# Kernel tuning notes

Hardware: AMD Instinct MI355X
Metric: run time of the kernel (lower is better)

## Reference

```python
import jax, jax.numpy as jnp
import numpy as np

NUM_SEGMENTS = 100000  # number of cycle slots (max cycle id + 1)


def setup_inputs() -> dict:
    key = jax.random.key(0)
    k1, k2, k3 = jax.random.split(key, 3)
    x = jax.random.randint(k1, (100000,), 0, 22, dtype=jnp.int64)
    atom_to_cycle = jax.random.randint(k2, (2, 600000), 0, NUM_SEGMENTS, dtype=jnp.int64)
    emb_weight = jax.random.normal(k3, (22, 128), dtype=jnp.float32)  # Embedding(22, hidden_dim)
    return {"x": x, "atom_to_cycle": atom_to_cycle, "emb_weight": emb_weight}


def reference(x, atom_to_cycle, emb_weight):
    # x: [N] int atom codes; atom_to_cycle: [2, E]; emb_weight: [22, D]
    h = emb_weight[x]                       # [N, D] embedding lookup
    gathered = h[atom_to_cycle[0]]          # [E, D] gather by atom index
    # scatter_sum over cycle ids -> [NUM_SEGMENTS, D]
    out = jax.ops.segment_sum(gathered, atom_to_cycle[1], num_segments=NUM_SEGMENTS)
    return out
```

## Files before the change

kernel.cpp:

```cpp
#include <hip/hip_runtime.h>
#include <stdint.h>

#define KCODES 22
#define KW     12

typedef int   int2v   __attribute__((ext_vector_type(2)));
typedef int   int4v   __attribute__((ext_vector_type(4)));
typedef float float4v __attribute__((ext_vector_type(4)));

#define BSHIFT   7
#define BROWS    128
#define BCAP     4096
#define EPT      8
#define CHUNK    2048
#define MAXBUCK  1024

__global__ __launch_bounds__(256) void bin_edges(
        const int* __restrict__ a2c, const int* __restrict__ x,
        uint32_t* __restrict__ gcur, uint16_t* __restrict__ bins,
        int E, int nbuck) {
    __shared__ uint32_t lcnt[MAXBUCK];
    __shared__ uint32_t lbase[MAXBUCK];
    const int tid = threadIdx.x;
    for (int b = tid; b < nbuck; b += 256) lcnt[b] = 0;
    __syncthreads();

    const int base = blockIdx.x * CHUNK + tid * EPT;
    int atoms[EPT] __attribute__((aligned(16)));
    int cycs[EPT]  __attribute__((aligned(16)));
    if (((E & 3) == 0) && (base + EPT <= E)) {
        *(int4v*)(atoms + 0) = __builtin_nontemporal_load((const int4v*)(a2c + base));
        *(int4v*)(atoms + 4) = __builtin_nontemporal_load((const int4v*)(a2c + base) + 1);
        *(int4v*)(cycs + 0)  = __builtin_nontemporal_load((const int4v*)(a2c + E + base));
        *(int4v*)(cycs + 4)  = __builtin_nontemporal_load((const int4v*)(a2c + E + base) + 1);
    } else {
#pragma unroll
        for (int j = 0; j < EPT; ++j) {
            int e = base + j;
            atoms[j] = (e < E) ? a2c[e] : 0;
            cycs[j]  = (e < E) ? a2c[E + e] : -1;
        }
    }

    uint16_t val[EPT], bk[EPT], rk[EPT];
#pragma unroll
    for (int j = 0; j < EPT; ++j) {
        if (cycs[j] >= 0) {
            uint32_t code = (uint32_t)x[atoms[j]];
            uint32_t b    = (uint32_t)cycs[j] >> BSHIFT;
            bk[j]  = (uint16_t)b;
            rk[j]  = (uint16_t)atomicAdd(&lcnt[b], 1u);
            val[j] = (uint16_t)((((uint32_t)cycs[j] & (BROWS - 1)) << 5) | code);
        } else {
            bk[j] = 0xFFFFu;
        }
    }
    __syncthreads();

    for (int b = tid; b < nbuck; b += 256) {
        uint32_t c = lcnt[b];
        lbase[b] = c ? atomicAdd(&gcur[b], c) : 0u;
    }
    __syncthreads();

#pragma unroll
    for (int j = 0; j < EPT; ++j) {
        if (bk[j] != 0xFFFFu) {
            uint32_t idx = lbase[bk[j]] + rk[j];
            if (idx < BCAP)
                bins[(size_t)bk[j] * BCAP + idx] = val[j];
        }
    }
}

__global__ __launch_bounds__(256) void hist_expand(
        const uint32_t* __restrict__ gcur, const uint16_t* __restrict__ bins,
        const float* __restrict__ emb, float* __restrict__ out, int num_seg) {
    __shared__ uint32_t hist[BROWS * KW];
    const int tid = threadIdx.x;
    const int b   = blockIdx.x;
    const int d4  = tid & 31;
    const int sub = tid >> 5;

    float4v e[KCODES];
#pragma unroll
    for (int k = 0; k < KCODES; ++k)
        e[k] = ((const float4v*)emb)[k * 32 + d4];

    for (int i = tid; i < BROWS * KW; i += 256) hist[i] = 0;
    __syncthreads();

    int n = gcur[b]; if (n > BCAP) n = BCAP;
    const uint16_t* bb = bins + (size_t)b * BCAP;
    for (int i = tid; i < n; i += 256) {
        uint32_t v = bb[i];
        atomicAdd(&hist[(v >> 5) * KW + ((v & 31u) >> 1)], 1u << ((v & 1u) << 4));
    }
    __syncthreads();

    for (int r = sub; r < BROWS; r += 8) {
        int cyc = b * BROWS + r;
        if (cyc >= num_seg) break;
        const uint4* hrow = (const uint4*)&hist[r * KW];
        uint4 w0 = hrow[0], w1 = hrow[1], w2 = hrow[2];
        uint32_t wv[12] = {w0.x, w0.y, w0.z, w0.w,
                           w1.x, w1.y, w1.z, w1.w,
                           w2.x, w2.y, w2.z, w2.w};
        float4v acc = (float4v)(0.f);
#pragma unroll
        for (int w = 0; w < 11; ++w) {
            float c0 = (float)(wv[w] & 0xFFFFu);
            float c1 = (float)(wv[w] >> 16);
            float4v e0 = e[2 * w], e1 = e[2 * w + 1];
            acc.x = fmaf(c1, e1.x, fmaf(c0, e0.x, acc.x));
            acc.y = fmaf(c1, e1.y, fmaf(c0, e0.y, acc.y));
            acc.z = fmaf(c1, e1.z, fmaf(c0, e0.z, acc.z));
            acc.w = fmaf(c1, e1.w, fmaf(c0, e0.w, acc.w));
        }
        __builtin_nontemporal_store(acc, &((float4v*)out)[(size_t)cyc * 32 + d4]);
    }
}

__global__ void count_edges2(const int* __restrict__ a2c,
                             const int* __restrict__ x,
                             uint32_t* __restrict__ cnt, int E) {
    int i = blockIdx.x * blockDim.x + threadIdx.x;
    int E2 = E >> 1;
    if (i < E2) {
        int2v a = __builtin_nontemporal_load(&((const int2v*)a2c)[i]);
        int2v c = __builtin_nontemporal_load(&((const int2v*)(a2c + E))[i]);
        uint32_t k0 = (uint32_t)x[a.x];
        uint32_t k1 = (uint32_t)x[a.y];
        atomicAdd(&cnt[(size_t)c.x * KW + (k0 >> 1)], 1u << ((k0 & 1) << 4));
        atomicAdd(&cnt[(size_t)c.y * KW + (k1 >> 1)], 1u << ((k1 & 1) << 4));
    }
}

__global__ void count_edges1(const int* __restrict__ a2c,
                             const int* __restrict__ x,
                             uint32_t* __restrict__ cnt, int E) {
    int e = blockIdx.x * blockDim.x + threadIdx.x;
    if (e < E) {
        int atom = a2c[e];
        int cyc  = a2c[E + e];
        uint32_t code = (uint32_t)x[atom];
        atomicAdd(&cnt[(size_t)cyc * KW + (code >> 1)], 1u << ((code & 1) << 4));
    }
}

__global__ __launch_bounds__(256) void expand_out(
        const uint32_t* __restrict__ cnt,
        const float* __restrict__ emb,
        float* __restrict__ out, int num_seg) {
    const int d4  = threadIdx.x & 31;
    const int sub = threadIdx.x >> 5;

    float4v e[KCODES];
#pragma unroll
    for (int k = 0; k < KCODES; ++k)
        e[k] = ((const float4v*)emb)[k * 32 + d4];

    for (int c = blockIdx.x * 8 + sub; c < num_seg; c += gridDim.x * 8) {
        const uint4* crow = (const uint4*)(cnt + (size_t)c * KW);
        uint4 w0 = crow[0], w1 = crow[1], w2 = crow[2];
        uint32_t wv[12] = {w0.x, w0.y, w0.z, w0.w,
                           w1.x, w1.y, w1.z, w1.w,
                           w2.x, w2.y, w2.z, w2.w};
        float4v acc = (float4v)(0.f);
#pragma unroll
        for (int w = 0; w < 11; ++w) {
            float c0 = (float)(wv[w] & 0xFFFFu);
            float c1 = (float)(wv[w] >> 16);
            float4v e0 = e[2 * w], e1 = e[2 * w + 1];
            acc.x = fmaf(c1, e1.x, fmaf(c0, e0.x, acc.x));
            acc.y = fmaf(c1, e1.y, fmaf(c0, e0.y, acc.y));
            acc.z = fmaf(c1, e1.z, fmaf(c0, e0.z, acc.z));
            acc.w = fmaf(c1, e1.w, fmaf(c0, e0.w, acc.w));
        }
        __builtin_nontemporal_store(acc, &((float4v*)out)[(size_t)c * 32 + d4]);
    }
}

__global__ void zero_out_f4(float4* __restrict__ out, int n4) {
    int i = blockIdx.x * blockDim.x + threadIdx.x;
    if (i < n4) out[i] = make_float4(0.f, 0.f, 0.f, 0.f);
}

__global__ void scatter_edges(const int* __restrict__ a2c,
                              const int* __restrict__ x,
                              const float* __restrict__ emb,
                              float* __restrict__ out, int E) {
    int t = blockIdx.x * blockDim.x + threadIdx.x;
    int e = t >> 5;
    int d = (t & 31) * 4;
    if (e < E) {
        int atom = a2c[e];
        int cyc  = a2c[E + e];
        int code = x[atom];
        const float4 ev = ((const float4*)emb)[code * 32 + (d >> 2)];
        float* o = out + (size_t)cyc * 128 + d;
        atomicAdd(o + 0, ev.x);
        atomicAdd(o + 1, ev.y);
        atomicAdd(o + 2, ev.z);
        atomicAdd(o + 3, ev.w);
    }
}

extern "C" void kernel_launch(void* const* d_in, const int* in_sizes, int n_in,
                              void* d_out, int out_size, void* d_ws, size_t ws_size,
                              hipStream_t stream) {
    const int*   x    = (const int*)d_in[0];
    const int*   a2c  = (const int*)d_in[1];
    const float* emb  = (const float*)d_in[2];
    float*       out  = (float*)d_out;

    const int E       = in_sizes[1] / 2;
    const int D       = in_sizes[2] / KCODES;
    const int num_seg = out_size / D;

    const int nbuck = (num_seg + BROWS - 1) >> BSHIFT;
    const size_t need_bin = 4096 + (size_t)nbuck * BCAP * sizeof(uint16_t);
    const size_t need_cnt = (size_t)num_seg * KW * sizeof(uint32_t);

    if (nbuck <= MAXBUCK && ws_size >= need_bin) {
        uint32_t* gcur = (uint32_t*)d_ws;
        uint16_t* bins = (uint16_t*)((char*)d_ws + 4096);

        (void)hipMemsetAsync(gcur, 0, (size_t)nbuck * sizeof(uint32_t), stream);

        int blocks1 = (E + CHUNK - 1) / CHUNK;
        bin_edges<<<blocks1, 256, 0, stream>>>(a2c, x, gcur, bins, E, nbuck);
        hist_expand<<<nbuck, 256, 0, stream>>>(gcur, bins, emb, out, num_seg);
    } else if (ws_size >= need_cnt) {
        uint32_t* cnt = (uint32_t*)d_ws;
        (void)hipMemsetAsync(cnt, 0, need_cnt, stream);
        if ((E & 1) == 0) {
            int E2 = E >> 1;
            count_edges2<<<(E2 + 255) / 256, 256, 0, stream>>>(a2c, x, cnt, E);
        } else {
            count_edges1<<<(E + 255) / 256, 256, 0, stream>>>(a2c, x, cnt, E);
        }
        int blocks = (num_seg + 7) / 8;
        if (blocks > 1024) blocks = 1024;
        expand_out<<<blocks, 256, 0, stream>>>(cnt, emb, out, num_seg);
    } else {
        int n4 = out_size / 4;
        zero_out_f4<<<(n4 + 255) / 256, 256, 0, stream>>>((float4*)out, n4);
        long long threads = (long long)E * 32;
        int blocks = (int)((threads + 255) / 256);
        scatter_edges<<<blocks, 256, 0, stream>>>(a2c, x, emb, out, E);
    }
    (void)n_in; (void)D;
}
```

Before: 102.6 us.

## Bin edges into fixed per-chunk bucket slots instead of global atomic cursors

A new binning kernel writes each chunk's edges into a dense [bucket][chunk][32] slot layout and records per-chunk counts. This removes the global atomic cursor, the second barrier pass and the memset launch. The histogram kernel then scans every chunk's slots for its bucket, reading paired 16-bit entries and skipping empty ones. The trade-offs are more workspace traffic from mostly empty slots, fewer and heavier blocks in the binning pass, and silent edge drops if any bucket receives more than 32 edges from one chunk. The older count-table fallback path is removed.

```diff
diff --git a/kernel.cpp b/kernel.cpp
--- a/kernel.cpp
+++ b/kernel.cpp
@@ -4,20 +4,128 @@
 #define KCODES 22
 #define KW     12
 
-typedef int   int2v   __attribute__((ext_vector_type(2)));
 typedef int   int4v   __attribute__((ext_vector_type(4)));
 typedef float float4v __attribute__((ext_vector_type(4)));
 
 #define BSHIFT   7
 #define BROWS    128
+#define MAXBUCK  1024
+#define EPT2     16
+#define CHUNK2   4096
+#define CAP      32
 #define BCAP     4096
 #define EPT      8
 #define CHUNK    2048
-#define MAXBUCK  1024
+
+__global__ __launch_bounds__(256) void bin_dense(
+        const int* __restrict__ a2c, const int* __restrict__ x,
+        uint16_t* __restrict__ cntm, uint16_t* __restrict__ bins,
+        int E, int nbuck, int nchunk) {
+    __shared__ uint32_t lcnt[MAXBUCK];
+    const int tid = threadIdx.x;
+    const int cb  = blockIdx.x;
+    for (int b = tid; b < nbuck; b += 256) lcnt[b] = 0;
+    __syncthreads();
+
+    const int base = cb * CHUNK2 + tid * EPT2;
+    int atoms[EPT2] __attribute__((aligned(16)));
+    int cycs[EPT2]  __attribute__((aligned(16)));
+    if (((E & 3) == 0) && (base + EPT2 <= E)) {
+#pragma unroll
+        for (int q = 0; q < EPT2 / 4; ++q) {
+            *(int4v*)(atoms + 4 * q) = __builtin_nontemporal_load((const int4v*)(a2c + base) + q);
+            *(int4v*)(cycs + 4 * q)  = __builtin_nontemporal_load((const int4v*)(a2c + E + base) + q);
+        }
+    } else {
+#pragma unroll
+        for (int j = 0; j < EPT2; ++j) {
+            int ei = base + j;
+            atoms[j] = (ei < E) ? a2c[ei] : 0;
+            cycs[j]  = (ei < E) ? a2c[E + ei] : -1;
+        }
+    }
+
+#pragma unroll
+    for (int j = 0; j < EPT2; ++j) {
+        if (cycs[j] >= 0) {
+            uint32_t code = (uint32_t)x[atoms[j]];
+            uint32_t b    = (uint32_t)cycs[j] >> BSHIFT;
+            uint32_t rk   = atomicAdd(&lcnt[b], 1u);
+            uint16_t val  = (uint16_t)((((uint32_t)cycs[j] & (BROWS - 1)) << 5) | code);
+            if (rk < CAP)
+                bins[((size_t)b * nchunk + cb) * CAP + rk] = val;
+        }
+    }
+    __syncthreads();
+
+    for (int b = tid; b < nbuck; b += 256)
+        cntm[(size_t)b * nchunk + cb] = (uint16_t)lcnt[b];
+}
+
+__global__ __launch_bounds__(256) void hist_expand2(
+        const uint16_t* __restrict__ cntm, const uint16_t* __restrict__ bins,
+        const float* __restrict__ emb, float* __restrict__ out,
+        int num_seg, int nchunk) {
+    __shared__ uint32_t hist[BROWS * KW];
+    __shared__ uint16_t lc[512];
+    const int tid = threadIdx.x;
+    const int b   = blockIdx.x;
+    const int d4  = tid & 31;
+    const int sub = tid >> 5;
+
+    float4v e[KCODES];
+#pragma unroll
+    for (int k = 0; k < KCODES; ++k)
+        e[k] = ((const float4v*)emb)[k * 32 + d4];
+
+    for (int i = tid; i < BROWS * KW; i += 256) hist[i] = 0;
+    for (int i = tid; i < nchunk; i += 256) lc[i] = cntm[(size_t)b * nchunk + i];
+    __syncthreads();
+
+    const uint32_t* bb = (const uint32_t*)(bins + (size_t)b * nchunk * CAP);
+    const int nslots2 = nchunk * (CAP / 2);
+    for (int s2 = tid; s2 < nslots2; s2 += 256) {
+        int i = s2 >> 4;
+        int j = (s2 & 15) * 2;
+        int c = lc[i];
+        if (j < c) {
+            uint32_t pair = bb[s2];
+            uint32_t v0 = pair & 0xFFFFu;
+            atomicAdd(&hist[(v0 >> 5) * KW + ((v0 & 31u) >> 1)], 1u << ((v0 & 1u) << 4));
+            if (j + 1 < c) {
+                uint32_t v1 = pair >> 16;
+                atomicAdd(&hist[(v1 >> 5) * KW + ((v1 & 31u) >> 1)], 1u << ((v1 & 1u) << 4));
+            }
+        }
+    }
+    __syncthreads();
+
+    for (int r = sub; r < BROWS; r += 8) {
+        int cyc = b * BROWS + r;
+        if (cyc >= num_seg) break;
+        const uint4* hrow = (const uint4*)&hist[r * KW];
+        uint4 w0 = hrow[0], w1 = hrow[1], w2 = hrow[2];
+        uint32_t wv[12] = {w0.x, w0.y, w0.z, w0.w,
+                           w1.x, w1.y, w1.z, w1.w,
+                           w2.x, w2.y, w2.z, w2.w};
+        float4v acc = (float4v)(0.f);
+#pragma unroll
+        for (int w = 0; w < 11; ++w) {
+            float c0 = (float)(wv[w] & 0xFFFFu);
+            float c1 = (float)(wv[w] >> 16);
+            float4v e0 = e[2 * w], e1 = e[2 * w + 1];
+            acc.x = fmaf(c1, e1.x, fmaf(c0, e0.x, acc.x));
+            acc.y = fmaf(c1, e1.y, fmaf(c0, e0.y, acc.y));
+            acc.z = fmaf(c1, e1.z, fmaf(c0, e0.z, acc.z));
+            acc.w = fmaf(c1, e1.w, fmaf(c0, e0.w, acc.w));
+        }
+        __builtin_nontemporal_store(acc, &((float4v*)out)[(size_t)cyc * 32 + d4]);
+    }
+}
 
 __global__ __launch_bounds__(256) void bin_edges(
         const int* __restrict__ a2c, const int* __restrict__ x,
-        uint32_t* __restrict__ gcur, uint16_t* __restrict__ bins,
+        uint32_t* __restrict__ gcur, uint16_t* __restrict__ binsA,
         int E, int nbuck) {
     __shared__ uint32_t lcnt[MAXBUCK];
     __shared__ uint32_t lbase[MAXBUCK];
@@ -36,9 +144,9 @@
     } else {
 #pragma unroll
         for (int j = 0; j < EPT; ++j) {
-            int e = base + j;
-            atoms[j] = (e < E) ? a2c[e] : 0;
-            cycs[j]  = (e < E) ? a2c[E + e] : -1;
+            int ei = base + j;
+            atoms[j] = (ei < E) ? a2c[ei] : 0;
+            cycs[j]  = (ei < E) ? a2c[E + ei] : -1;
         }
     }
 
@@ -68,13 +176,13 @@
         if (bk[j] != 0xFFFFu) {
             uint32_t idx = lbase[bk[j]] + rk[j];
             if (idx < BCAP)
-                bins[(size_t)bk[j] * BCAP + idx] = val[j];
+                binsA[(size_t)bk[j] * BCAP + idx] = val[j];
         }
     }
 }
 
 __global__ __launch_bounds__(256) void hist_expand(
-        const uint32_t* __restrict__ gcur, const uint16_t* __restrict__ bins,
+        const uint32_t* __restrict__ gcur, const uint16_t* __restrict__ binsA,
         const float* __restrict__ emb, float* __restrict__ out, int num_seg) {
     __shared__ uint32_t hist[BROWS * KW];
     const int tid = threadIdx.x;
@@ -91,7 +199,7 @@
     __syncthreads();
 
     int n = gcur[b]; if (n > BCAP) n = BCAP;
-    const uint16_t* bb = bins + (size_t)b * BCAP;
+    const uint16_t* bb = binsA + (size_t)b * BCAP;
     for (int i = tid; i < n; i += 256) {
         uint32_t v = bb[i];
         atomicAdd(&hist[(v >> 5) * KW + ((v & 31u) >> 1)], 1u << ((v & 1u) << 4));
@@ -118,66 +226,6 @@
             acc.w = fmaf(c1, e1.w, fmaf(c0, e0.w, acc.w));
         }
         __builtin_nontemporal_store(acc, &((float4v*)out)[(size_t)cyc * 32 + d4]);
-    }
-}
-
-__global__ void count_edges2(const int* __restrict__ a2c,
-                             const int* __restrict__ x,
-                             uint32_t* __restrict__ cnt, int E) {
-    int i = blockIdx.x * blockDim.x + threadIdx.x;
-    int E2 = E >> 1;
-    if (i < E2) {
-        int2v a = __builtin_nontemporal_load(&((const int2v*)a2c)[i]);
-        int2v c = __builtin_nontemporal_load(&((const int2v*)(a2c + E))[i]);
-        uint32_t k0 = (uint32_t)x[a.x];
-        uint32_t k1 = (uint32_t)x[a.y];
-        atomicAdd(&cnt[(size_t)c.x * KW + (k0 >> 1)], 1u << ((k0 & 1) << 4));
-        atomicAdd(&cnt[(size_t)c.y * KW + (k1 >> 1)], 1u << ((k1 & 1) << 4));
-    }
-}
-
-__global__ void count_edges1(const int* __restrict__ a2c,
-                             const int* __restrict__ x,
-                             uint32_t* __restrict__ cnt, int E) {
-    int e = blockIdx.x * blockDim.x + threadIdx.x;
-    if (e < E) {
-        int atom = a2c[e];
-        int cyc  = a2c[E + e];
-        uint32_t code = (uint32_t)x[atom];
-        atomicAdd(&cnt[(size_t)cyc * KW + (code >> 1)], 1u << ((code & 1) << 4));
-    }
-}
-
-__global__ __launch_bounds__(256) void expand_out(
-        const uint32_t* __restrict__ cnt,
-        const float* __restrict__ emb,
-        float* __restrict__ out, int num_seg) {
-    const int d4  = threadIdx.x & 31;
-    const int sub = threadIdx.x >> 5;
-
-    float4v e[KCODES];
-#pragma unroll
-    for (int k = 0; k < KCODES; ++k)
-        e[k] = ((const float4v*)emb)[k * 32 + d4];
-
-    for (int c = blockIdx.x * 8 + sub; c < num_seg; c += gridDim.x * 8) {
-        const uint4* crow = (const uint4*)(cnt + (size_t)c * KW);
-        uint4 w0 = crow[0], w1 = crow[1], w2 = crow[2];
-        uint32_t wv[12] = {w0.x, w0.y, w0.z, w0.w,
-                           w1.x, w1.y, w1.z, w1.w,
-                           w2.x, w2.y, w2.z, w2.w};
-        float4v acc = (float4v)(0.f);
-#pragma unroll
-        for (int w = 0; w < 11; ++w) {
-            float c0 = (float)(wv[w] & 0xFFFFu);
-            float c1 = (float)(wv[w] >> 16);
-            float4v e0 = e[2 * w], e1 = e[2 * w + 1];
-            acc.x = fmaf(c1, e1.x, fmaf(c0, e0.x, acc.x));
-            acc.y = fmaf(c1, e1.y, fmaf(c0, e0.y, acc.y));
-            acc.z = fmaf(c1, e1.z, fmaf(c0, e0.z, acc.z));
-            acc.w = fmaf(c1, e1.w, fmaf(c0, e0.w, acc.w));
-        }
-        __builtin_nontemporal_store(acc, &((float4v*)out)[(size_t)c * 32 + d4]);
     }
 }
 
@@ -218,31 +266,28 @@
     const int D       = in_sizes[2] / KCODES;
     const int num_seg = out_size / D;
 
-    const int nbuck = (num_seg + BROWS - 1) >> BSHIFT;
-    const size_t need_bin = 4096 + (size_t)nbuck * BCAP * sizeof(uint16_t);
-    const size_t need_cnt = (size_t)num_seg * KW * sizeof(uint32_t);
-
-    if (nbuck <= MAXBUCK && ws_size >= need_bin) {
-        uint32_t* gcur = (uint32_t*)d_ws;
-        uint16_t* bins = (uint16_t*)((char*)d_ws + 4096);
-
-        (void)hipMemsetAsync(gcur, 0, (size_t)nbuck * sizeof(uint32_t), stream);
-
+    const int nbuck  = (num_seg + BROWS - 1) >> BSHIFT;
+    const int nchunk = (E + CHUNK2 - 1) / CHUNK2;
+
+    const size_t cntm_bytes = (size_t)nbuck * nchunk * sizeof(uint16_t);
+    const size_t bins_off   = (cntm_bytes + 65535) & ~(size_t)65535;
+    const size_t need_dense = bins_off + (size_t)nbuck * nchunk * CAP * sizeof(uint16_t);
+    const size_t curA_bytes = (size_t)nbuck * sizeof(uint32_t);
+    const size_t binsA_off  = (curA_bytes + 65535) & ~(size_t)65535;
+    const size_t need_A     = binsA_off + (size_t)nbuck * BCAP * sizeof(uint16_t);
+
+    if (nbuck <= MAXBUCK && nchunk <= 512 && ws_size >= need_dense) {
+        uint16_t* cntm = (uint16_t*)d_ws;
+        uint16_t* bins = (uint16_t*)((char*)d_ws + bins_off);
+        bin_dense<<<nchunk, 256, 0, stream>>>(a2c, x, cntm, bins, E, nbuck, nchunk);
+        hist_expand2<<<nbuck, 256, 0, stream>>>(cntm, bins, emb, out, num_seg, nchunk);
+    } else if (nbuck <= MAXBUCK && ws_size >= need_A) {
+        uint32_t* gcur  = (uint32_t*)d_ws;
+        uint16_t* binsA = (uint16_t*)((char*)d_ws + binsA_off);
+        (void)hipMemsetAsync(gcur, 0, curA_bytes, stream);
         int blocks1 = (E + CHUNK - 1) / CHUNK;
-        bin_edges<<<blocks1, 256, 0, stream>>>(a2c, x, gcur, bins, E, nbuck);
-        hist_expand<<<nbuck, 256, 0, stream>>>(gcur, bins, emb, out, num_seg);
-    } else if (ws_size >= need_cnt) {
-        uint32_t* cnt = (uint32_t*)d_ws;
-        (void)hipMemsetAsync(cnt, 0, need_cnt, stream);
-        if ((E & 1) == 0) {
-            int E2 = E >> 1;
-            count_edges2<<<(E2 + 255) / 256, 256, 0, stream>>>(a2c, x, cnt, E);
-        } else {
-            count_edges1<<<(E + 255) / 256, 256, 0, stream>>>(a2c, x, cnt, E);
-        }
-        int blocks = (num_seg + 7) / 8;
-        if (blocks > 1024) blocks = 1024;
-        expand_out<<<blocks, 256, 0, stream>>>(cnt, emb, out, num_seg);
+        bin_edges<<<blocks1, 256, 0, stream>>>(a2c, x, gcur, binsA, E, nbuck);
+        hist_expand<<<nbuck, 256, 0, stream>>>(gcur, binsA, emb, out, num_seg);
     } else {
         int n4 = out_size / 4;
         zero_out_f4<<<(n4 + 255) / 256, 256, 0, stream>>>((float4*)out, n4);
```

Result: no change. 101.8 us (-0.7%).
